# Kernel tuning notes

Measured on AMD Instinct MI355X. Metric: run time of the kernel, lower is better.

Reference implementation:

```python
import jax, jax.numpy as jnp
import numpy as np

B, C, T = 8, 512, 4096
KC, VC, H = 512, 512, 1  # key_channels, value_channels, num_heads
SCALE = KC // (H ** 0.5)  # faithful to original: key_channels // num_heads**0.5


def setup_inputs() -> dict:
    key = jax.random.key(0)
    k1, k2, k3, k4, k5 = jax.random.split(key, 5)
    x = jax.random.normal(k1, (B, C, T), dtype=jnp.float32)
    # 1x1 Conv1d weights: Conv1d(C, out, kernel_size=1) == per-timestep Linear
    Wqk = jax.random.normal(k2, (KC, C), dtype=jnp.float32) / np.sqrt(C)
    bqk = jax.random.normal(k3, (KC,), dtype=jnp.float32) * 0.01
    Wv = jax.random.normal(k4, (VC, C), dtype=jnp.float32) / np.sqrt(C)
    bv = jax.random.normal(k5, (VC,), dtype=jnp.float32) * 0.01
    return {"x": x, "Wqk": Wqk, "bqk": bqk, "Wv": Wv, "bv": bv}


def reference(x, Wqk, bqk, Wv, bv):
    # 1x1 conv projections: [B,C,T] -> [B,K,T] / [B,V,T]
    qk = jnp.einsum('kc,bct->bkt', Wqk, x) + bqk[None, :, None]
    val = jnp.einsum('vc,bct->bvt', Wv, x) + bv[None, :, None]
    # channel-wise attention: with num_heads=1 the reshape/transpose/matmul
    # chain reduces to scores[b,k,v] = sum_t qk[b,k,t] * val[b,v,t]
    scores = jnp.einsum('bkt,bvt->bkv', qk, val) / SCALE
    p = jax.nn.softmax(scores, axis=-1)          # softmax over value channels
    # inference path: dropout is identity (self.training == False)
    out = jnp.einsum('bkv,bvt->bkt', p, val)     # [B,K,T], K == input_channels
    return out.reshape(-1, C, T)
```

## Files before the change

kernel.cpp:

```cpp
#include <hip/hip_runtime.h>
#include <hip/hip_bf16.h>


#define BB 8
#define CC 512
#define TT 4096

typedef __attribute__((ext_vector_type(8))) short bf16x8;
typedef __attribute__((ext_vector_type(4))) short bf16x4;
typedef __attribute__((ext_vector_type(4))) float f32x4;

__device__ __forceinline__ void gload_lds16(const void* g, void* l) {
  __builtin_amdgcn_global_load_lds((const __attribute__((address_space(1))) void*)g,
                                   (__attribute__((address_space(3))) void*)l,
                                   16, 0, 0);
}
__device__ __forceinline__ float bf2f(short u) {
  return __uint_as_float(((unsigned)(unsigned short)u) << 16);
}
__device__ __forceinline__ unsigned short f2bf(float f) {
  return __builtin_bit_cast(unsigned short, __float2bfloat16(f));
}
__device__ __forceinline__ void bar_fence() {
  asm volatile("" ::: "memory");
  __builtin_amdgcn_s_barrier();
  asm volatile("" ::: "memory");
}
__device__ __forceinline__ void bar_lds() {
  asm volatile("s_waitcnt lgkmcnt(0)" ::: "memory");
  __builtin_amdgcn_s_barrier();
  asm volatile("" ::: "memory");
}

__global__ __launch_bounds__(256)
void convert_stream_kernel(const float* __restrict__ x, __hip_bfloat16* __restrict__ xh,
                           float* __restrict__ sx)
{
  const int gid = blockIdx.x * 256 + threadIdx.x;
#pragma unroll
  for (int it = 0; it < 4; it++) {
    const int chunk = it * 524288 + gid;
    const size_t base = (size_t)chunk * 8;
    const float4 a = *(const float4*)&x[base];
    const float4 c = *(const float4*)&x[base + 4];
    bf16x8 h;
    h[0] = (short)f2bf(a.x); h[1] = (short)f2bf(a.y);
    h[2] = (short)f2bf(a.z); h[3] = (short)f2bf(a.w);
    h[4] = (short)f2bf(c.x); h[5] = (short)f2bf(c.y);
    h[6] = (short)f2bf(c.z); h[7] = (short)f2bf(c.w);
    *(bf16x8*)&xh[base] = h;
    float s = ((a.x + a.y) + (a.z + a.w)) + ((c.x + c.y) + (c.z + c.w));
#pragma unroll
    for (int off = 32; off; off >>= 1) s += __shfl_xor(s, off);
    if ((threadIdx.x & 63) == 0) atomicAdd(&sx[chunk >> 9], s);
  }
}

__global__ __launch_bounds__(256)
void prep_w_kernel(const float* __restrict__ Wqk, const float* __restrict__ Wv,
                   const float* __restrict__ sx,
                   __hip_bfloat16* __restrict__ Wqkh, __hip_bfloat16* __restrict__ Wvh,
                   __hip_bfloat16* __restrict__ WvT,
                   float* __restrict__ ta, float* __restrict__ tb)
{
  const int blk = blockIdx.x;
  if (blk < 1024) {
    int i = blk * 256 + threadIdx.x;
    Wqkh[i] = __float2bfloat16(Wqk[i]);
    float wv = Wv[i];
    Wvh[i] = __float2bfloat16(wv);
    WvT[(i & 511) * 512 + (i >> 9)] = __float2bfloat16(wv);
  } else {
    int wid = threadIdx.x >> 6, lane = threadIdx.x & 63;
    int gid = (blk - 1024) * 4 + wid;
    int which = gid >> 12;
    int rem = gid & 4095;
    int b = rem >> 9, j = rem & 511;
    const float* W = which ? Wv : Wqk;
    float s = 0.f;
#pragma unroll
    for (int i2 = 0; i2 < 8; i2++) {
      int c = lane + i2 * 64;
      s += W[j * 512 + c] * sx[b * 512 + c];
    }
#pragma unroll
    for (int off = 32; off; off >>= 1) s += __shfl_xor(s, off);
    if (lane == 0) (which ? tb : ta)[b * 512 + j] = s;
  }
}

template <int BM, int BN>
__global__ __launch_bounds__(256)
void gemm_nt_kernel(const __hip_bfloat16* __restrict__ A, long strideA, int ldA,
                    const __hip_bfloat16* __restrict__ B, long strideB, int ldB,
                    void* __restrict__ C, long strideC, int ldC,
                    int Kslice, int nslices)
{
  static_assert(BM == 128 && BN == 128, "vmcnt(8) count assumes 8 loads/stage");
  constexpr int FM = BM / 32, FN = BN / 32;
  const int tid = threadIdx.x, lane = tid & 63, wid = tid >> 6;

  const int gx = gridDim.x, gy = gridDim.y;
  const int lin = blockIdx.x + gx * (blockIdx.y + gy * blockIdx.z);
  const int nwg = gx * gy * (int)gridDim.z;
  const int lin2 = (lin & 7) * (nwg >> 3) + (lin >> 3);
  const int tn = lin2 % gx;
  const int r1 = lin2 / gx;
  const int tm = r1 % gy;
  const int z  = r1 / gy;
  const int b  = z / nslices;
  const int ks = z - b * nslices;

  const __hip_bfloat16* Ab = A + (size_t)b * strideA + (size_t)(tm * BM) * ldA + (size_t)ks * Kslice;
  const __hip_bfloat16* Bb = B + (size_t)b * strideB + (size_t)(tn * BN) * ldB + (size_t)ks * Kslice;

  __shared__ __align__(16) __hip_bfloat16 sA[2][BM * 64];
  __shared__ __align__(16) __hip_bfloat16 sB[2][BN * 64];

  const int wr = wid >> 1, wc = wid & 1;

  f32x4 acc[FM][FN];
#pragma unroll
  for (int m = 0; m < FM; m++)
#pragma unroll
    for (int n = 0; n < FN; n++) acc[m][n] = (f32x4){0.f, 0.f, 0.f, 0.f};

  auto stage = [&](int buf, int k0) {
#pragma unroll
    for (int i = 0; i < BM / 32; i++) {
      int e = tid * 8 + i * 2048;
      int row = e >> 6, colg = (e & 63) ^ ((row & 7) << 3);
      gload_lds16(Ab + (size_t)row * ldA + k0 + colg, &sA[buf][wid * 512 + i * 2048]);
    }
#pragma unroll
    for (int i = 0; i < BN / 32; i++) {
      int e = tid * 8 + i * 2048;
      int row = e >> 6, colg = (e & 63) ^ ((row & 7) << 3);
      gload_lds16(Bb + (size_t)row * ldB + k0 + colg, &sB[buf][wid * 512 + i * 2048]);
    }
  };

  const int nsteps = Kslice >> 6;
  stage(0, 0);
  if (nsteps > 1) stage(1, 64);
#pragma unroll 1
  for (int s = 0; s < nsteps; s++) {
    if (s + 1 < nsteps) asm volatile("s_waitcnt vmcnt(8)" ::: "memory");
    else                asm volatile("s_waitcnt vmcnt(0)" ::: "memory");
    bar_fence();
    const __hip_bfloat16* cA = sA[s & 1];
    const __hip_bfloat16* cB = sB[s & 1];
#pragma unroll
    for (int ks2 = 0; ks2 < 2; ks2++) {
      bf16x8 af[FM], bfv[FN];
      const int kb = ks2 * 32 + (lane >> 4) * 8;
#pragma unroll
      for (int m = 0; m < FM; m++) {
        int row = wr * (BM / 2) + m * 16 + (lane & 15);
        af[m] = *(const bf16x8*)&cA[row * 64 + (kb ^ ((row & 7) << 3))];
      }
#pragma unroll
      for (int n = 0; n < FN; n++) {
        int row = wc * (BN / 2) + n * 16 + (lane & 15);
        bfv[n] = *(const bf16x8*)&cB[row * 64 + (kb ^ ((row & 7) << 3))];
      }
#pragma unroll
      for (int m = 0; m < FM; m++)
#pragma unroll
        for (int n = 0; n < FN; n++)
          acc[m][n] = __builtin_amdgcn_mfma_f32_16x16x32_bf16(af[m], bfv[n], acc[m][n], 0, 0, 0);
    }
    bar_fence();
    if (s + 2 < nsteps) stage(s & 1, (s + 2) << 6);
  }

  const int rb = tm * BM + wr * (BM / 2) + ((lane >> 4) << 2);
  const int cb = tn * BN + wc * (BN / 2) + (lane & 15);
  __hip_bfloat16* Cb = (__hip_bfloat16*)C + (size_t)z * strideC;
#pragma unroll
  for (int m = 0; m < FM; m++)
#pragma unroll
    for (int n = 0; n < FN; n++)
#pragma unroll
      for (int r = 0; r < 4; r++) {
        int row = rb + m * 16 + r, col = cb + n * 16;
        Cb[(size_t)row * ldC + col] = __float2bfloat16(acc[m][n][r]);
      }
}

__global__ __launch_bounds__(256)
void reduce_g_kernel(const short* __restrict__ Gpart, short* __restrict__ Gb)
{
  const int idx = (blockIdx.x * 256 + threadIdx.x) * 8;
  const int b = idx >> 18, i = idx & 262143;
  const short* base = Gpart + ((size_t)(b * 8) << 18) + i;
  float s[8];
#pragma unroll
  for (int q = 0; q < 8; q++) s[q] = 0.f;
#pragma unroll
  for (int ks = 0; ks < 8; ks++) {
    bf16x8 v = *(const bf16x8*)(base + ((size_t)ks << 18));
#pragma unroll
    for (int q = 0; q < 8; q++) s[q] += bf2f(v[q]);
  }
  bf16x8 o;
#pragma unroll
  for (int q = 0; q < 8; q++) o[q] = (short)f2bf(s[q]);
  *(bf16x8*)(Gb + ((size_t)b << 18) + i) = o;
}

__global__ __launch_bounds__(256)
void middle_kernel(const __hip_bfloat16* __restrict__ Gh,
                   const __hip_bfloat16* __restrict__ Wqkh,
                   const __hip_bfloat16* __restrict__ Wvh,
                   const __hip_bfloat16* __restrict__ WvT,
                   const float* __restrict__ bqk, const float* __restrict__ bv,
                   const float* __restrict__ ta, const float* __restrict__ tb,
                   __hip_bfloat16* __restrict__ Mm, float* __restrict__ pb)
{
  __shared__ __align__(16) __hip_bfloat16 sT[16 * 512];
  __shared__ float red1[4][16], red2[4][16], red3[4][16];

  const int tid = threadIdx.x, lane = tid & 63, wid = tid >> 6;
  const int lin = blockIdx.x;
  const int lin2 = (lin & 7) * 32 + (lin >> 3);
  const int strip = lin2 & 31, b = lin2 >> 5;
  const __hip_bfloat16* Ghb = Gh + (size_t)b * 262144;

  const int arow = lane & 15;
  const int asw = (arow & 7) << 3;
  const int kb = (lane >> 4) * 8;
  const size_t browK = (size_t)(wid * 128 + (lane & 15)) * 512;
  f32x4 acc[8];

#define RUN16(AF_EXPR, BSRC)                                                    \
  {                                                                             \
    _Pragma("unroll") for (int n = 0; n < 8; n++) acc[n] = (f32x4){0.f,0.f,0.f,0.f}; \
    _Pragma("unroll") for (int t = 0; t < 16; t++) {                            \
      const int kq = t * 32 + kb;                                               \
      bf16x8 af = (AF_EXPR);                                                    \
      _Pragma("unroll") for (int n = 0; n < 8; n++) {                           \
        bf16x8 bfv = *(const bf16x8*)&(BSRC)[browK + (size_t)n * 16 * 512 + kq];\
        acc[n] = __builtin_amdgcn_mfma_f32_16x16x32_bf16(af, bfv, acc[n], 0, 0, 0); \
      }                                                                         \
    }                                                                           \
  }

  const __hip_bfloat16* Aq = Wqkh + (size_t)(strip * 16 + arow) * 512;
  RUN16(*(const bf16x8*)&Aq[kq], Ghb);
#pragma unroll
  for (int n = 0; n < 8; n++)
#pragma unroll
    for (int r = 0; r < 4; r++) {
      int lr = ((lane >> 4) << 2) + r;
      int col = wid * 128 + n * 16 + (lane & 15);
      sT[lr * 512 + (col ^ ((lr & 7) << 3))] = __float2bfloat16(acc[n][r]);
    }
  bar_lds();

  RUN16(*(const bf16x8*)&sT[arow * 512 + (kq ^ asw)], Wvh);

  const float* tab = ta + b * 512;
  const float* tbb = tb + b * 512;
  float bvc[8], tbc[8];
#pragma unroll
  for (int n = 0; n < 8; n++) {
    int col = wid * 128 + n * 16 + (lane & 15);
    bvc[n] = bv[col]; tbc[n] = tbb[col];
  }
  float bq[4], tar[4];
#pragma unroll
  for (int r = 0; r < 4; r++) {
    int gr = strip * 16 + ((lane >> 4) << 2) + r;
    bq[r] = bqk[gr]; tar[r] = tab[gr];
  }
#pragma unroll
  for (int n = 0; n < 8; n++)
#pragma unroll
    for (int r = 0; r < 4; r++)
      acc[n][r] = (acc[n][r] + bq[r] * tbc[n] + tar[r] * bvc[n]
                   + 4096.0f * bq[r] * bvc[n]) * (1.0f / 512.0f);

#pragma unroll
  for (int r = 0; r < 4; r++) {
    float v = acc[0][r];
#pragma unroll
    for (int n = 1; n < 8; n++) v = fmaxf(v, acc[n][r]);
#pragma unroll
    for (int off = 1; off < 16; off <<= 1) v = fmaxf(v, __shfl_xor(v, off));
    if ((lane & 15) == 0) red1[wid][((lane >> 4) << 2) + r] = v;
  }
  bar_lds();
  float mx[4];
#pragma unroll
  for (int r = 0; r < 4; r++) {
    int lr = ((lane >> 4) << 2) + r;
    mx[r] = fmaxf(fmaxf(red1[0][lr], red1[1][lr]), fmaxf(red1[2][lr], red1[3][lr]));
  }
#pragma unroll
  for (int r = 0; r < 4; r++) {
    float s = 0.f, pp = 0.f;
#pragma unroll
    for (int n = 0; n < 8; n++) {
      float e = __expf(acc[n][r] - mx[r]);
      acc[n][r] = e;
      s += e; pp += e * bvc[n];
    }
#pragma unroll
    for (int off = 1; off < 16; off <<= 1) { s += __shfl_xor(s, off); pp += __shfl_xor(pp, off); }
    if ((lane & 15) == 0) {
      red2[wid][((lane >> 4) << 2) + r] = s;
      red3[wid][((lane >> 4) << 2) + r] = pp;
    }
  }
  bar_lds();
  float inv[4];
#pragma unroll
  for (int r = 0; r < 4; r++) {
    int lr = ((lane >> 4) << 2) + r;
    float sum = red2[0][lr] + red2[1][lr] + red2[2][lr] + red2[3][lr];
    inv[r] = 1.0f / sum;
    if (wid == 0 && (lane & 15) == 0)
      pb[b * 512 + strip * 16 + lr] =
          (red3[0][lr] + red3[1][lr] + red3[2][lr] + red3[3][lr]) * inv[r];
  }
#pragma unroll
  for (int n = 0; n < 8; n++)
#pragma unroll
    for (int r = 0; r < 4; r++) {
      int lr = ((lane >> 4) << 2) + r;
      int col = wid * 128 + n * 16 + (lane & 15);
      sT[lr * 512 + (col ^ ((lr & 7) << 3))] = __float2bfloat16(acc[n][r] * inv[r]);
    }
  bar_lds();

  RUN16(*(const bf16x8*)&sT[arow * 512 + (kq ^ asw)], WvT);
#undef RUN16

  __hip_bfloat16* Mb = Mm + (size_t)b * 262144 + (size_t)(strip * 16) * 512;
#pragma unroll
  for (int n = 0; n < 8; n++)
#pragma unroll
    for (int r = 0; r < 4; r++) {
      int lr = ((lane >> 4) << 2) + r;
      int col = wid * 128 + n * 16 + (lane & 15);
      Mb[(size_t)lr * 512 + col] = __float2bfloat16(acc[n][r]);
    }
}

__global__ __launch_bounds__(256)
void gemm_out_kernel(const __hip_bfloat16* __restrict__ Mall,
                     const __hip_bfloat16* __restrict__ xh,
                     const float* __restrict__ pball,
                     float* __restrict__ out)
{
  __shared__ __align__(16) __hip_bfloat16 sA[2][128 * 64];
  __shared__ __align__(16) __hip_bfloat16 sB[2][64 * 128];

  const int tid = threadIdx.x, lane = tid & 63, wid = tid >> 6;
  const int wr = wid >> 1, wc = wid & 1;

  const int lin = blockIdx.x + 32 * (blockIdx.y + 4 * blockIdx.z);
  const int lin2 = (lin & 7) * 128 + (lin >> 3);
  const int tm = lin2 & 3;
  const int tn = (lin2 >> 2) & 31;
  const int b  = lin2 >> 7;

  const __hip_bfloat16* Ab = Mall + (size_t)b * 262144 + (size_t)(tm * 128) * 512;
  const __hip_bfloat16* Bb = xh + (size_t)b * ((size_t)CC * TT) + tn * 128;

  f32x4 acc[4][4];
#pragma unroll
  for (int m = 0; m < 4; m++)
#pragma unroll
    for (int n = 0; n < 4; n++) acc[m][n] = (f32x4){0.f, 0.f, 0.f, 0.f};

  auto stage = [&](int buf, int k0) {
#pragma unroll
    for (int i = 0; i < 4; i++) {
      int e = tid * 8 + i * 2048;
      int row = e >> 6, colg = (e & 63) ^ ((row & 7) << 3);
      gload_lds16(Ab + (size_t)row * 512 + k0 + colg, &sA[buf][wid * 512 + i * 2048]);
    }
#pragma unroll
    for (int q = 0; q < 4; q++) {
      int E = q * 2048 + tid * 8;
      int v = ((E >> 9) << 2) | ((E >> 4) & 3);
      int t = (((E >> 6) & 7) << 4) | (E & 8);
      gload_lds16(Bb + (size_t)(k0 + v) * TT + t, &sB[buf][wid * 512 + q * 2048]);
    }
  };

  const unsigned sB32 =
      (unsigned)(size_t)(__attribute__((address_space(3))) __hip_bfloat16*)&sB[0][0];
  const unsigned btr_lo = sB32 + (lane >> 4) * 2048 + (lane & 15) * 8 + wc * 512;
  const unsigned btr_hi = btr_lo + 8192;

#define COMPUTE(BUF)                                                            \
  {                                                                             \
    _Pragma("unroll")                                                           \
    for (int ks2 = 0; ks2 < 2; ks2++) {                                         \
      bf16x8 af[4]; bf16x4 blo[4], bhi[4];                                      \
      const int kb = ks2 * 32 + (lane >> 4) * 8;                                \
      _Pragma("unroll")                                                         \
      for (int m = 0; m < 4; m++) {                                             \
        int row = wr * 64 + m * 16 + (lane & 15);                               \
        af[m] = *(const bf16x8*)&sA[BUF][row * 64 + (kb ^ ((row & 7) << 3))];   \
      }                                                                         \
      unsigned ab = ks2 ? btr_hi : btr_lo;                                      \
      _Pragma("unroll")                                                         \
      for (int n = 0; n < 4; n++) {                                             \
        asm volatile("ds_read_b64_tr_b16 %0, %1 offset:%2"                      \
                     : "=v"(blo[n]) : "v"(ab), "i"((BUF) * 16384 + n * 128));   \
        asm volatile("ds_read_b64_tr_b16 %0, %1 offset:%2"                      \
                     : "=v"(bhi[n]) : "v"(ab), "i"((BUF) * 16384 + n * 128 + 1024)); \
      }                                                                         \
      asm volatile("s_waitcnt lgkmcnt(0)" ::: "memory");                        \
      __builtin_amdgcn_sched_barrier(0);                                        \
      _Pragma("unroll")                                                         \
      for (int m = 0; m < 4; m++)                                               \
        _Pragma("unroll")                                                       \
        for (int n = 0; n < 4; n++) {                                           \
          bf16x8 b8 = __builtin_shufflevector(blo[n], bhi[n], 0, 1, 2, 3, 4, 5, 6, 7); \
          acc[m][n] = __builtin_amdgcn_mfma_f32_16x16x32_bf16(af[m], b8, acc[m][n], 0, 0, 0); \
        }                                                                       \
    }                                                                           \
  }

  stage(0, 0);
  stage(1, 64);
#pragma unroll 1
  for (int s = 0; s < 8; s += 2) {
    asm volatile("s_waitcnt vmcnt(8)" ::: "memory");
    bar_fence();
    COMPUTE(0);
    bar_fence();
    if (s + 2 < 8) stage(0, (s + 2) * 64);
    if (s + 2 < 8) asm volatile("s_waitcnt vmcnt(8)" ::: "memory");
    else           asm volatile("s_waitcnt vmcnt(0)" ::: "memory");
    bar_fence();
    COMPUTE(1);
    bar_fence();
    if (s + 3 < 8) stage(1, (s + 3) * 64);
  }
#undef COMPUTE

  const int rb = tm * 128 + wr * 64 + ((lane >> 4) << 2);
  const int cb = tn * 128 + wc * 64 + (lane & 15);
  float* Cf = out + (size_t)b * ((size_t)CC * TT);
  const float* pbv = pball + b * 512;
#pragma unroll
  for (int m = 0; m < 4; m++)
#pragma unroll
    for (int n = 0; n < 4; n++)
#pragma unroll
      for (int r = 0; r < 4; r++) {
        int row = rb + m * 16 + r, col = cb + n * 16;
        Cf[(size_t)row * TT + col] = acc[m][n][r] + pbv[row];
      }
}

extern "C" void kernel_launch(void* const* d_in, const int* in_sizes, int n_in,
                              void* d_out, int out_size, void* d_ws, size_t ws_size,
                              hipStream_t stream)
{
  const float* x   = (const float*)d_in[0];
  const float* Wqk = (const float*)d_in[1];
  const float* bqk = (const float*)d_in[2];
  const float* Wv  = (const float*)d_in[3];
  const float* bv  = (const float*)d_in[4];
  float* out = (float*)d_out;

  char* w = (char*)d_ws;
  auto alloc = [&](size_t bytes) {
    void* pp = (void*)w;
    w += (bytes + 255) & ~(size_t)255;
    return pp;
  };
  __hip_bfloat16* xh     = (__hip_bfloat16*)alloc((size_t)BB * CC * TT * 2);
  short*          Gpart  = (short*)alloc((size_t)BB * 8 * CC * CC * 2);
  short*          Gb     = (short*)alloc((size_t)BB * CC * CC * 2);
  __hip_bfloat16* Mm     = (__hip_bfloat16*)alloc((size_t)BB * CC * CC * 2);
  __hip_bfloat16* Wqkh   = (__hip_bfloat16*)alloc((size_t)CC * CC * 2);
  __hip_bfloat16* Wvh    = (__hip_bfloat16*)alloc((size_t)CC * CC * 2);
  __hip_bfloat16* WvT    = (__hip_bfloat16*)alloc((size_t)CC * CC * 2);
  float* sx = (float*)alloc((size_t)BB * CC * 4);
  float* ta = (float*)alloc((size_t)BB * CC * 4);
  float* tb = (float*)alloc((size_t)BB * CC * 4);
  float* pb = (float*)alloc((size_t)BB * CC * 4);

  hipMemsetAsync(sx, 0, (size_t)BB * CC * 4, stream);

  convert_stream_kernel<<<2048, 256, 0, stream>>>(x, xh, sx);
  prep_w_kernel<<<3072, 256, 0, stream>>>(Wqk, Wv, sx, Wqkh, Wvh, WvT, ta, tb);

  const long sXH = (long)CC * TT;
  const long sSq = (long)CC * CC;

  gemm_nt_kernel<128, 128><<<dim3(4, 4, BB * 8), 256, 0, stream>>>(
      xh, sXH, TT, xh, sXH, TT, Gpart, sSq, CC, 512, 8);
  reduce_g_kernel<<<(BB * CC * CC) / (256 * 8), 256, 0, stream>>>(Gpart, Gb);

  middle_kernel<<<256, 256, 0, stream>>>(
      (const __hip_bfloat16*)Gb, Wqkh, Wvh, WvT, bqk, bv, ta, tb, Mm, pb);

  gemm_out_kernel<<<dim3(32, 4, 8), 256, 0, stream>>>(Mm, xh, pb, out);
}
```

Before: 231.8 us.

## Exploit Gram symmetry in xxᵀ GEMM and pipeline middle kernel B-operand via LDS

The Gram GEMM now computes only the 10 upper-triangular 128x128 tiles per batch/slice (640 blocks instead of 1024). The reduce kernel sums those tiles and mirrors the off-diagonal ones into the lower triangle with transposed scalar stores. The middle kernel now stages its B operands (G, Wv, WvT) through a 4-deep LDS ring with async global-to-LDS loads and keeps the A fragments in registers, replacing direct global loads per MFMA. This trades more LDS use and uncoalesced transposed writes for less GEMM work and better latency hiding.

```diff
diff --git a/kernel.cpp b/kernel.cpp
--- a/kernel.cpp
+++ b/kernel.cpp
@@ -89,102 +89,94 @@
   }
 }
 
-template <int BM, int BN>
 __global__ __launch_bounds__(256)
-void gemm_nt_kernel(const __hip_bfloat16* __restrict__ A, long strideA, int ldA,
-                    const __hip_bfloat16* __restrict__ B, long strideB, int ldB,
-                    void* __restrict__ C, long strideC, int ldC,
-                    int Kslice, int nslices)
-{
-  static_assert(BM == 128 && BN == 128, "vmcnt(8) count assumes 8 loads/stage");
-  constexpr int FM = BM / 32, FN = BN / 32;
+void gemm_gram_kernel(const __hip_bfloat16* __restrict__ xh, short* __restrict__ Gpart)
+{
   const int tid = threadIdx.x, lane = tid & 63, wid = tid >> 6;
-
-  const int gx = gridDim.x, gy = gridDim.y;
-  const int lin = blockIdx.x + gx * (blockIdx.y + gy * blockIdx.z);
-  const int nwg = gx * gy * (int)gridDim.z;
-  const int lin2 = (lin & 7) * (nwg >> 3) + (lin >> 3);
-  const int tn = lin2 % gx;
-  const int r1 = lin2 / gx;
-  const int tm = r1 % gy;
-  const int z  = r1 / gy;
-  const int b  = z / nslices;
-  const int ks = z - b * nslices;
-
-  const __hip_bfloat16* Ab = A + (size_t)b * strideA + (size_t)(tm * BM) * ldA + (size_t)ks * Kslice;
-  const __hip_bfloat16* Bb = B + (size_t)b * strideB + (size_t)(tn * BN) * ldB + (size_t)ks * Kslice;
-
-  __shared__ __align__(16) __hip_bfloat16 sA[2][BM * 64];
-  __shared__ __align__(16) __hip_bfloat16 sB[2][BN * 64];
+  const int lin = blockIdx.x;
+  const int lin2 = (lin & 7) * 80 + (lin >> 3);
+  const int t = lin2 % 10;
+  const int z = lin2 / 10;
+  int tm, tn;
+  if (t < 4)      { tm = 0; tn = t; }
+  else if (t < 7) { tm = 1; tn = t - 3; }
+  else if (t < 9) { tm = 2; tn = t - 5; }
+  else            { tm = 3; tn = 3; }
+  const int b = z >> 3, ks = z & 7;
+
+  const __hip_bfloat16* Ab = xh + (size_t)b * CC * TT + (size_t)(tm * 128) * TT + ks * 512;
+  const __hip_bfloat16* Bb = xh + (size_t)b * CC * TT + (size_t)(tn * 128) * TT + ks * 512;
+
+  __shared__ __align__(16) __hip_bfloat16 sA[2][128 * 64];
+  __shared__ __align__(16) __hip_bfloat16 sB[2][128 * 64];
 
   const int wr = wid >> 1, wc = wid & 1;
 
-  f32x4 acc[FM][FN];
-#pragma unroll
-  for (int m = 0; m < FM; m++)
-#pragma unroll
-    for (int n = 0; n < FN; n++) acc[m][n] = (f32x4){0.f, 0.f, 0.f, 0.f};
+  f32x4 acc[4][4];
+#pragma unroll
+  for (int m = 0; m < 4; m++)
+#pragma unroll
+    for (int n = 0; n < 4; n++) acc[m][n] = (f32x4){0.f, 0.f, 0.f, 0.f};
 
   auto stage = [&](int buf, int k0) {
 #pragma unroll
-    for (int i = 0; i < BM / 32; i++) {
+    for (int i = 0; i < 4; i++) {
       int e = tid * 8 + i * 2048;
       int row = e >> 6, colg = (e & 63) ^ ((row & 7) << 3);
-      gload_lds16(Ab + (size_t)row * ldA + k0 + colg, &sA[buf][wid * 512 + i * 2048]);
-    }
-#pragma unroll
-    for (int i = 0; i < BN / 32; i++) {
+      gload_lds16(Ab + (size_t)row * TT + k0 + colg, &sA[buf][wid * 512 + i * 2048]);
+    }
+#pragma unroll
+    for (int i = 0; i < 4; i++) {
       int e = tid * 8 + i * 2048;
       int row = e >> 6, colg = (e & 63) ^ ((row & 7) << 3);
-      gload_lds16(Bb + (size_t)row * ldB + k0 + colg, &sB[buf][wid * 512 + i * 2048]);
+      gload_lds16(Bb + (size_t)row * TT + k0 + colg, &sB[buf][wid * 512 + i * 2048]);
     }
   };
 
-  const int nsteps = Kslice >> 6;
   stage(0, 0);
-  if (nsteps > 1) stage(1, 64);
+  stage(1, 64);
 #pragma unroll 1
-  for (int s = 0; s < nsteps; s++) {
-    if (s + 1 < nsteps) asm volatile("s_waitcnt vmcnt(8)" ::: "memory");
-    else                asm volatile("s_waitcnt vmcnt(0)" ::: "memory");
+  for (int s = 0; s < 8; s++) {
+    if (s + 1 < 8) asm volatile("s_waitcnt vmcnt(8)" ::: "memory");
+    else           asm volatile("s_waitcnt vmcnt(0)" ::: "memory");
     bar_fence();
     const __hip_bfloat16* cA = sA[s & 1];
     const __hip_bfloat16* cB = sB[s & 1];
 #pragma unroll
     for (int ks2 = 0; ks2 < 2; ks2++) {
-      bf16x8 af[FM], bfv[FN];
+      bf16x8 af[4], bfv[4];
       const int kb = ks2 * 32 + (lane >> 4) * 8;
 #pragma unroll
-      for (int m = 0; m < FM; m++) {
-        int row = wr * (BM / 2) + m * 16 + (lane & 15);
+      for (int m = 0; m < 4; m++) {
+        int row = wr * 64 + m * 16 + (lane & 15);
         af[m] = *(const bf16x8*)&cA[row * 64 + (kb ^ ((row & 7) << 3))];
       }
 #pragma unroll
-      for (int n = 0; n < FN; n++) {
-        int row = wc * (BN / 2) + n * 16 + (lane & 15);
+      for (int n = 0; n < 4; n++) {
+        int row = wc * 64 + n * 16 + (lane & 15);
         bfv[n] = *(const bf16x8*)&cB[row * 64 + (kb ^ ((row & 7) << 3))];
       }
 #pragma unroll
-      for (int m = 0; m < FM; m++)
-#pragma unroll
-        for (int n = 0; n < FN; n++)
+      for (int m = 0; m < 4; m++)
+#pragma unroll
+        for (int n = 0; n < 4; n++)
           acc[m][n] = __builtin_amdgcn_mfma_f32_16x16x32_bf16(af[m], bfv[n], acc[m][n], 0, 0, 0);
     }
     bar_fence();
-    if (s + 2 < nsteps) stage(s & 1, (s + 2) << 6);
-  }
-
-  const int rb = tm * BM + wr * (BM / 2) + ((lane >> 4) << 2);
-  const int cb = tn * BN + wc * (BN / 2) + (lane & 15);
-  __hip_bfloat16* Cb = (__hip_bfloat16*)C + (size_t)z * strideC;
-#pragma unroll
-  for (int m = 0; m < FM; m++)
-#pragma unroll
-    for (int n = 0; n < FN; n++)
+    if (s + 2 < 8) stage(s & 1, (s + 2) << 6);
+  }
+
+  const int rb = tm * 128 + wr * 64 + ((lane >> 4) << 2);
+  const int cb = tn * 128 + wc * 64 + (lane & 15);
+  __hip_bfloat16* Cb = (__hip_bfloat16*)Gpart + (size_t)z * 262144;
+#pragma unroll
+  for (int m = 0; m < 4; m++)
+#pragma unroll
+    for (int n = 0; n < 4; n++)
 #pragma unroll
       for (int r = 0; r < 4; r++) {
         int row = rb + m * 16 + r, col = cb + n * 16;
-        Cb[(size_t)row * ldC + col] = __float2bfloat16(acc[m][n][r]);
+        Cb[(size_t)row * 512 + col] = __float2bfloat16(acc[m][n][r]);
       }
 }
 
@@ -193,6 +185,8 @@
 {
   const int idx = (blockIdx.x * 256 + threadIdx.x) * 8;
   const int b = idx >> 18, i = idx & 262143;
+  const int row = i >> 9, col = i & 511;
+  if ((col >> 7) < (row >> 7)) return;
   const short* base = Gpart + ((size_t)(b * 8) << 18) + i;
   float s[8];
 #pragma unroll
@@ -207,6 +201,11 @@
 #pragma unroll
   for (int q = 0; q < 8; q++) o[q] = (short)f2bf(s[q]);
   *(bf16x8*)(Gb + ((size_t)b << 18) + i) = o;
+  if ((col >> 7) > (row >> 7)) {
+#pragma unroll
+    for (int q = 0; q < 8; q++)
+      Gb[((size_t)b << 18) + (size_t)(col + q) * 512 + row] = o[q];
+  }
 }
 
 __global__ __launch_bounds__(256)
@@ -218,6 +217,7 @@
                    const float* __restrict__ ta, const float* __restrict__ tb,
                    __hip_bfloat16* __restrict__ Mm, float* __restrict__ pb)
 {
+  __shared__ __align__(16) __hip_bfloat16 sB[4][512 * 32];
   __shared__ __align__(16) __hip_bfloat16 sT[16 * 512];
   __shared__ float red1[4][16], red2[4][16], red3[4][16];
 
@@ -230,24 +230,61 @@
   const int arow = lane & 15;
   const int asw = (arow & 7) << 3;
   const int kb = (lane >> 4) * 8;
-  const size_t browK = (size_t)(wid * 128 + (lane & 15)) * 512;
+
+  bf16x8 af_all[16];
+  {
+    const __hip_bfloat16* Aq = Wqkh + (size_t)(strip * 16 + arow) * 512;
+#pragma unroll
+    for (int t = 0; t < 16; t++) af_all[t] = *(const bf16x8*)&Aq[t * 32 + kb];
+  }
+  asm volatile("" ::: "memory");
+
+  auto stageB = [&](int buf, int gt) {
+    const __hip_bfloat16* Bsrc = (gt < 16) ? Ghb : (gt < 32 ? Wvh : WvT);
+    const int k0 = (gt & 15) * 32;
+#pragma unroll
+    for (int i = 0; i < 8; i++) {
+      int r = i * 64 + wid * 16 + (lane >> 2);
+      int scol = k0 + 8 * ((lane & 3) ^ ((r >> 1) & 3));
+      gload_lds16(Bsrc + (size_t)r * 512 + scol, &sB[buf][i * 2048 + wid * 512]);
+    }
+  };
+
+  stageB(0, 0); stageB(1, 1); stageB(2, 2); stageB(3, 3);
+
   f32x4 acc[8];
 
-#define RUN16(AF_EXPR, BSRC)                                                    \
+#define HALF(GT, AF)                                                            \
   {                                                                             \
-    _Pragma("unroll") for (int n = 0; n < 8; n++) acc[n] = (f32x4){0.f,0.f,0.f,0.f}; \
-    _Pragma("unroll") for (int t = 0; t < 16; t++) {                            \
-      const int kq = t * 32 + kb;                                               \
-      bf16x8 af = (AF_EXPR);                                                    \
-      _Pragma("unroll") for (int n = 0; n < 8; n++) {                           \
-        bf16x8 bfv = *(const bf16x8*)&(BSRC)[browK + (size_t)n * 16 * 512 + kq];\
-        acc[n] = __builtin_amdgcn_mfma_f32_16x16x32_bf16(af, bfv, acc[n], 0, 0, 0); \
-      }                                                                         \
+    const __hip_bfloat16* cB = sB[(GT) & 3];                                    \
+    bf16x8 af = (AF);                                                           \
+    _Pragma("unroll") for (int n = 0; n < 8; n++) {                             \
+      int brow = wid * 128 + n * 16 + (lane & 15);                              \
+      bf16x8 bfv = *(const bf16x8*)&cB[brow * 32 + (kb ^ (((brow >> 1) & 3) << 3))]; \
+      acc[n] = __builtin_amdgcn_mfma_f32_16x16x32_bf16(af, bfv, acc[n], 0, 0, 0); \
     }                                                                           \
   }
 
-  const __hip_bfloat16* Aq = Wqkh + (size_t)(strip * 16 + arow) * 512;
-  RUN16(*(const bf16x8*)&Aq[kq], Ghb);
+#define PAIR(GT, AF0, AF1)                                                      \
+  {                                                                             \
+    if ((GT) < 46) asm volatile("s_waitcnt vmcnt(16)" ::: "memory");            \
+    else           asm volatile("s_waitcnt vmcnt(0)" ::: "memory");             \
+    bar_fence();                                                                \
+    __builtin_amdgcn_s_setprio(1);                                              \
+    HALF(GT, AF0);                                                              \
+    HALF((GT) + 1, AF1);                                                        \
+    __builtin_amdgcn_s_setprio(0);                                              \
+    bar_fence();                                                                \
+    if ((GT) + 4 <= 47) stageB(((GT) + 4) & 3, (GT) + 4);                       \
+    if ((GT) + 5 <= 47) stageB(((GT) + 5) & 3, (GT) + 5);                       \
+  }
+
+#define LDT(T) (*(const bf16x8*)&sT[arow * 512 + ((((T) * 32) + kb) ^ asw)])
+
+#pragma unroll
+  for (int n = 0; n < 8; n++) acc[n] = (f32x4){0.f, 0.f, 0.f, 0.f};
+#pragma unroll
+  for (int p = 0; p < 8; p++) PAIR(2 * p, af_all[2 * p], af_all[2 * p + 1]);
 #pragma unroll
   for (int n = 0; n < 8; n++)
 #pragma unroll
@@ -258,7 +295,10 @@
     }
   bar_lds();
 
-  RUN16(*(const bf16x8*)&sT[arow * 512 + (kq ^ asw)], Wvh);
+#pragma unroll
+  for (int n = 0; n < 8; n++) acc[n] = (f32x4){0.f, 0.f, 0.f, 0.f};
+#pragma unroll
+  for (int p = 0; p < 8; p++) PAIR(16 + 2 * p, LDT(2 * p), LDT(2 * p + 1));
 
   const float* tab = ta + b * 512;
   const float* tbb = tb + b * 512;
@@ -334,8 +374,14 @@
     }
   bar_lds();
 
-  RUN16(*(const bf16x8*)&sT[arow * 512 + (kq ^ asw)], WvT);
-#undef RUN16
+#pragma unroll
+  for (int n = 0; n < 8; n++) acc[n] = (f32x4){0.f, 0.f, 0.f, 0.f};
+#pragma unroll
+  for (int p = 0; p < 8; p++) PAIR(32 + 2 * p, LDT(2 * p), LDT(2 * p + 1));
+
+#undef PAIR
+#undef HALF
+#undef LDT
 
   __hip_bfloat16* Mb = Mm + (size_t)b * 262144 + (size_t)(strip * 16) * 512;
 #pragma unroll
@@ -494,11 +540,7 @@
   convert_stream_kernel<<<2048, 256, 0, stream>>>(x, xh, sx);
   prep_w_kernel<<<3072, 256, 0, stream>>>(Wqk, Wv, sx, Wqkh, Wvh, WvT, ta, tb);
 
-  const long sXH = (long)CC * TT;
-  const long sSq = (long)CC * CC;
-
-  gemm_nt_kernel<128, 128><<<dim3(4, 4, BB * 8), 256, 0, stream>>>(
-      xh, sXH, TT, xh, sXH, TT, Gpart, sSq, CC, 512, 8);
+  gemm_gram_kernel<<<640, 256, 0, stream>>>(xh, Gpart);
   reduce_g_kernel<<<(BB * CC * CC) / (256 * 8), 256, 0, stream>>>(Gpart, Gb);
 
   middle_kernel<<<256, 256, 0, stream>>>(
```

New measurement: 223.0 us. -3.8%, faster.
